# Performance work log

Measured on AMD Instinct MI355X. Metric: run time of the kernel, lower is better.

The kernel has to match this reference:

```python
import jax, jax.numpy as jnp
import numpy as np

N = 50000        # nodes
E = 800000       # edges
D_IN = 128       # input feature dim (== 2*hidden)
H = 64           # hidden_dim
G = 64           # graphs in batch
BN_EPS = 1e-5


def setup_inputs() -> dict:
    key = jax.random.key(0)
    ks = jax.random.split(key, 8)
    x = jax.random.normal(ks[0], (N, D_IN), jnp.float32)
    edge_index = jax.random.randint(ks[1], (2, E), 0, N, dtype=jnp.int32)
    edge_attribute = jax.random.normal(ks[2], (E,), jnp.float32)
    batch = jnp.sort(jax.random.randint(ks[3], (N,), 0, G, dtype=jnp.int32))
    # 7 GIN layers; all first linears are [D_IN=2H -> H]
    W1 = jax.random.normal(ks[4], (7, D_IN, H), jnp.float32) * (1.0 / np.sqrt(D_IN))
    bn1_g = jnp.ones((7, H), jnp.float32)
    bn1_b = jnp.zeros((7, H), jnp.float32)
    # layers 0..5 second linear [H -> 2H] + BN
    W2 = jax.random.normal(ks[5], (6, H, 2 * H), jnp.float32) * (1.0 / np.sqrt(H))
    bn2_g = jnp.ones((6, 2 * H), jnp.float32)
    bn2_b = jnp.zeros((6, 2 * H), jnp.float32)
    # layer 6 second linear [H -> 2], no BN
    W_last = jax.random.normal(ks[6], (H, 2), jnp.float32) * (1.0 / np.sqrt(H))
    eps = jnp.zeros((7,), jnp.float32)  # train_eps=True, init 0
    return dict(x=x, edge_index=edge_index, edge_attribute=edge_attribute,
                batch=batch, W1=W1, bn1_g=bn1_g, bn1_b=bn1_b, W2=W2,
                bn2_g=bn2_g, bn2_b=bn2_b, W_last=W_last, eps=eps)


def _bn(h, g, b):
    # training-mode BatchNorm1d over node axis, biased variance
    mu = h.mean(0)
    var = h.var(0)
    return g * (h - mu) * jax.lax.rsqrt(var + BN_EPS) + b


def reference(x, edge_index, edge_attribute, batch, W1, bn1_g, bn1_b, W2,
              bn2_g, bn2_b, W_last, eps):
    src, dst = edge_index[0], edge_index[1]
    for i in range(7):
        # GIN aggregation: sum of neighbor features (edge_attribute unused)
        agg = jax.ops.segment_sum(x[src], dst, num_segments=N)
        h = (1.0 + eps[i]) * x + agg
        h = jax.nn.relu(_bn(h @ W1[i], bn1_g[i], bn1_b[i]))
        if i < 6:
            h = _bn(h @ W2[i], bn2_g[i], bn2_b[i])
        else:
            h = h @ W_last
        # F.dropout treated as identity (deterministic eval); then ReLU
        x = jax.nn.relu(h)
    # global_mean_pool over graphs
    counts = jax.ops.segment_sum(jnp.ones((N,), x.dtype), batch, num_segments=G)
    sums = jax.ops.segment_sum(x, batch, num_segments=G)
    return sums / jnp.maximum(counts, 1.0)[:, None]
```

## Files before the change

kernel.cpp:

```cpp
#include <hip/hip_runtime.h>
#include <hip/hip_fp16.h>

#define NN 50000
#define EE 800000
#define GG 64
#define BNEPS 1e-5f

typedef _Float16 f16x8 __attribute__((ext_vector_type(8)));
typedef _Float16 f16x2 __attribute__((ext_vector_type(2)));
typedef float f32x4 __attribute__((ext_vector_type(4)));

__device__ inline float2 h2f(unsigned int u) {
    __half2 h = __builtin_bit_cast(__half2, u);
    return __half22float2(h);
}
__device__ inline unsigned int f2h(float a, float b) {
    __half2 h = __float22half2_rn(make_float2(a, b));
    return __builtin_bit_cast(unsigned int, h);
}
__device__ inline __half2 relu2(__half2 v) {
    const __half z = __float2half(0.f);
    return __halves2half2(__hmax(__low2half(v), z), __hmax(__high2half(v), z));
}
__device__ inline float acc_lo(unsigned int u, float c) {
    return __builtin_amdgcn_fdot2(__builtin_bit_cast(f16x2, u), f16x2{(_Float16)1.f, (_Float16)0.f}, c, false);
}
__device__ inline float acc_hi(unsigned int u, float c) {
    return __builtin_amdgcn_fdot2(__builtin_bit_cast(f16x2, u), f16x2{(_Float16)0.f, (_Float16)1.f}, c, false);
}


__global__ void hist_kernel(const int* __restrict__ ei, int* __restrict__ deg) {
    int e = blockIdx.x * 256 + threadIdx.x;
    if (e < EE) atomicAdd(&deg[ei[EE + e]], 1);
}

__global__ void scan1_kernel(const int* __restrict__ deg, int* __restrict__ offs,
                             int* __restrict__ bsum) {
    __shared__ int lds[1024];
    int i = blockIdx.x * 1024 + threadIdx.x;
    int v = (i < NN) ? deg[i] : 0;
    lds[threadIdx.x] = v;
    __syncthreads();
    for (int d = 1; d < 1024; d <<= 1) {
        int t = (threadIdx.x >= d) ? lds[threadIdx.x - d] : 0;
        __syncthreads();
        lds[threadIdx.x] += t;
        __syncthreads();
    }
    int incl = lds[threadIdx.x];
    if (i < NN) offs[i] = incl - v;
    if (threadIdx.x == 1023) bsum[blockIdx.x] = incl;
}

__global__ void scan3_kernel(int* __restrict__ offs, int* __restrict__ cursor,
                             const int* __restrict__ bsum) {
    __shared__ int base;
    if (threadIdx.x == 0) {
        int r = 0;
        for (int b = 0; b < (int)blockIdx.x; ++b) r += bsum[b];
        base = r;
    }
    __syncthreads();
    int i = blockIdx.x * 1024 + threadIdx.x;
    if (i < NN) {
        int o = offs[i] + base;
        offs[i] = o;
        cursor[i] = o;
    }
    if (i == 0 && blockIdx.x == 0) offs[NN] = EE;
}

__global__ void scatter_kernel(const int* __restrict__ ei, int* __restrict__ cursor,
                               unsigned short* __restrict__ srcs) {
    int e = blockIdx.x * 256 + threadIdx.x;
    if (e < EE) {
        int s = ei[e];
        int d = ei[EE + e];
        int pos = atomicAdd(&cursor[d], 1);
        srcs[pos] = (unsigned short)s;
    }
}


__global__ void cvt_kernel(const float* __restrict__ in, __half* __restrict__ out) {
    int i = blockIdx.x * 256 + threadIdx.x;
    if (i >= NN * 16) return;
    const float4* p = (const float4*)in + i * 2;
    float4 a = p[0], b = p[1];
    uint4 o;
    o.x = f2h(a.x, a.y);
    o.y = f2h(a.z, a.w);
    o.z = f2h(b.x, b.y);
    o.w = f2h(b.z, b.w);
    ((uint4*)out)[i] = o;
}


__global__ void packW_kernel(const float* __restrict__ W, __half* __restrict__ Wpk, int K,
                             int C, int layers) {
    int NKF = K / 32, NCF = C / 16;
    int per_layer = NKF * NCF * 64;
    int t = blockIdx.x * 256 + threadIdx.x;
    if (t >= layers * per_layer) return;
    int layer = t / per_layer, r = t % per_layer;
    int kf = r / (NCF * 64), r2 = r % (NCF * 64);
    int cf = r2 >> 6, l = r2 & 63;
    const float* Wl = W + (size_t)layer * K * C;
    __half* o = Wpk + ((size_t)layer * per_layer + ((size_t)(kf * NCF + cf) * 64 + l)) * 8;
    int k0 = kf * 32 + (l >> 4) * 8, c = cf * 16 + (l & 15);
#pragma unroll
    for (int j = 0; j < 8; ++j) o[j] = __float2half(Wl[(size_t)(k0 + j) * C + c]);
}


__global__ __launch_bounds__(256) void bnrelu_kernel(__half* __restrict__ a,
                                                     const float* __restrict__ stats,
                                                     const float* __restrict__ bg,
                                                     const float* __restrict__ bb) {
    __shared__ float lsc[128], lsh[128];
    if (threadIdx.x < 128) {
        int c = threadIdx.x;
        float mu = stats[c] * (1.0f / NN);
        float var = stats[128 + c] * (1.0f / NN) - mu * mu;
        float inv = rsqrtf(var + BNEPS);
        float sc = bg[c] * inv;
        lsc[c] = sc;
        lsh[c] = bb[c] - mu * sc;
    }
    __syncthreads();
    const int total = NN * 16;
    for (int t = blockIdx.x * 256 + threadIdx.x; t < total; t += gridDim.x * 256) {
        uint4 u = ((const uint4*)a)[t];
        int c0 = (t & 15) * 8;
        unsigned int* up = &u.x;
        uint4 o;
        unsigned int* op = &o.x;
#pragma unroll
        for (int j = 0; j < 4; ++j) {
            float2 f = h2f(up[j]);
            f.x = fmaxf(fmaf(f.x, lsc[c0 + 2 * j], lsh[c0 + 2 * j]), 0.f);
            f.y = fmaxf(fmaf(f.y, lsc[c0 + 2 * j + 1], lsh[c0 + 2 * j + 1]), 0.f);
            op[j] = f2h(f.x, f.y);
        }
        ((uint4*)a)[t] = o;
    }
}


__global__ __launch_bounds__(256) void agg_kernel(const __half* __restrict__ x,
                                                  const int* __restrict__ offs,
                                                  const unsigned short* __restrict__ srcs,
                                                  const float* __restrict__ epsp, int layer,
                                                  __half* __restrict__ h0) {
    int node = blockIdx.x * 4 + (threadIdx.x >> 6);
    if (node >= NN) return;
    int lane = threadIdx.x & 63;
    int g = lane >> 3;
    int l = lane & 7;
    float acc[16];
#pragma unroll
    for (int j = 0; j < 16; ++j) acc[j] = 0.f;

    int beg = offs[node], end = offs[node + 1];
    int i0 = beg + g, i1 = i0 + 8;
    int s0 = (i0 < end) ? (int)srcs[i0] : 0;
    int s1 = (i1 < end) ? (int)srcs[i1] : 0;
    const uint4* r0 = (const uint4*)(x + (size_t)s0 * 128) + l * 2;
    const uint4* r1 = (const uint4*)(x + (size_t)s1 * 128) + l * 2;
    uint4 va = r0[0], vb = r0[1];
    uint4 wa = r1[0], wb = r1[1];
    const uint4* sp = (const uint4*)(x + (size_t)node * 128) + l * 2;
    uint4 xa, xb;
    if (g == 0) {
        xa = sp[0];
        xb = sp[1];
    }
    for (int base = beg; base + g < end; base += 8) {
        int i2 = base + 16 + g;
        int sP = (i2 < end) ? (int)srcs[i2] : 0;
        const uint4* r2 = (const uint4*)(x + (size_t)sP * 128) + l * 2;
        uint4 ua = r2[0], ub = r2[1];
#pragma unroll
        for (int j = 0; j < 8; ++j) {
            unsigned int u = (j == 0) ? va.x : (j == 1) ? va.y : (j == 2) ? va.z
                             : (j == 3) ? va.w : (j == 4) ? vb.x : (j == 5) ? vb.y
                             : (j == 6) ? vb.z : vb.w;
            acc[2 * j] = acc_lo(u, acc[2 * j]);
            acc[2 * j + 1] = acc_hi(u, acc[2 * j + 1]);
        }
        va = wa; vb = wb;
        wa = ua; wb = ub;
    }
    float e1 = 1.0f + epsp[layer];
    if (g == 0) {
#pragma unroll
        for (int j = 0; j < 8; ++j) {
            unsigned int u = (j == 0) ? xa.x : (j == 1) ? xa.y : (j == 2) ? xa.z
                             : (j == 3) ? xa.w : (j == 4) ? xb.x : (j == 5) ? xb.y
                             : (j == 6) ? xb.z : xb.w;
            float2 f = h2f(u);
            acc[2 * j] = fmaf(e1, f.x, acc[2 * j]);
            acc[2 * j + 1] = fmaf(e1, f.y, acc[2 * j + 1]);
        }
    }
#pragma unroll
    for (int d = 8; d < 64; d <<= 1)
#pragma unroll
        for (int j = 0; j < 16; ++j) acc[j] += __shfl_xor(acc[j], d);
    if (g == 0) {
        uint4 o0, o1;
        o0.x = f2h(acc[0], acc[1]);
        o0.y = f2h(acc[2], acc[3]);
        o0.z = f2h(acc[4], acc[5]);
        o0.w = f2h(acc[6], acc[7]);
        o1.x = f2h(acc[8], acc[9]);
        o1.y = f2h(acc[10], acc[11]);
        o1.z = f2h(acc[12], acc[13]);
        o1.w = f2h(acc[14], acc[15]);
        uint4* o = (uint4*)(h0 + (size_t)node * 128 + l * 16);
        o[0] = o0;
        o[1] = o1;
    }
}


__global__ __launch_bounds__(256) void gemm1_kernel(const __half* __restrict__ h0,
                                                    const __half* __restrict__ Wpk,
                                                    __half* __restrict__ y,
                                                    float* __restrict__ stats) {
    int lane = threadIdx.x & 63, wave = threadIdx.x >> 6, g = lane >> 4;
    f16x8 bf[4][4];
    const f16x8* wp = (const f16x8*)Wpk;
#pragma unroll
    for (int kf = 0; kf < 4; ++kf)
#pragma unroll
        for (int cf = 0; cf < 4; ++cf) bf[kf][cf] = wp[(kf * 4 + cf) * 64 + lane];
    float s[4] = {0.f, 0.f, 0.f, 0.f}, s2[4] = {0.f, 0.f, 0.f, 0.f};
    for (int tile = blockIdx.x * 4 + wave; tile < NN / 16; tile += gridDim.x * 4) {
        int node16 = tile * 16;
        f32x4 acc[4];
#pragma unroll
        for (int cf = 0; cf < 4; ++cf) acc[cf] = (f32x4){0.f, 0.f, 0.f, 0.f};
        const f16x8* xr = (const f16x8*)(h0 + (size_t)(node16 + (lane & 15)) * 128);
#pragma unroll
        for (int kf = 0; kf < 4; ++kf) {
            f16x8 af = xr[kf * 4 + g];
#pragma unroll
            for (int cf = 0; cf < 4; ++cf)
                acc[cf] =
                    __builtin_amdgcn_mfma_f32_16x16x32_f16(af, bf[kf][cf], acc[cf], 0, 0, 0);
        }
#pragma unroll
        for (int cf = 0; cf < 4; ++cf) {
#pragma unroll
            for (int r = 0; r < 4; ++r) {
                float v = acc[cf][r];
                float p = __shfl_xor(v, 1);
                if (!(lane & 1)) {
                    int node = node16 + g * 4 + r;
                    int ch = cf * 16 + (lane & 15);
                    *(unsigned int*)(y + (size_t)node * 64 + ch) = f2h(v, p);
                }
                s[cf] += v;
                s2[cf] += v * v;
            }
        }
    }
#pragma unroll
    for (int d = 16; d < 64; d <<= 1)
#pragma unroll
        for (int cf = 0; cf < 4; ++cf) {
            s[cf] += __shfl_xor(s[cf], d);
            s2[cf] += __shfl_xor(s2[cf], d);
        }
    __shared__ float lst[4][128];
    if (lane < 16) {
#pragma unroll
        for (int cf = 0; cf < 4; ++cf) {
            lst[wave][cf * 16 + lane] = s[cf];
            lst[wave][64 + cf * 16 + lane] = s2[cf];
        }
    }
    __syncthreads();
    if (threadIdx.x < 128)
        atomicAdd(&stats[threadIdx.x], lst[0][threadIdx.x] + lst[1][threadIdx.x] +
                                           lst[2][threadIdx.x] + lst[3][threadIdx.x]);
}


__global__ __launch_bounds__(256) void gemm2_kernel(const __half* __restrict__ y1,
                                                    const __half* __restrict__ Wpk,
                                                    const float* __restrict__ stats1,
                                                    const float* __restrict__ bg,
                                                    const float* __restrict__ bb,
                                                    __half* __restrict__ y2,
                                                    float* __restrict__ stats2) {
    __shared__ __half2 lsc2[32], lsh2[32];
    if (threadIdx.x < 32) {
        int p = threadIdx.x;
        int c0 = 2 * p, c1 = 2 * p + 1;
        float mu0 = stats1[c0] * (1.0f / NN);
        float var0 = stats1[64 + c0] * (1.0f / NN) - mu0 * mu0;
        float is0 = rsqrtf(var0 + BNEPS);
        float sc0 = bg[c0] * is0;
        float mu1 = stats1[c1] * (1.0f / NN);
        float var1 = stats1[64 + c1] * (1.0f / NN) - mu1 * mu1;
        float is1 = rsqrtf(var1 + BNEPS);
        float sc1 = bg[c1] * is1;
        lsc2[p] = __floats2half2_rn(sc0, sc1);
        lsh2[p] = __floats2half2_rn(bb[c0] - mu0 * sc0, bb[c1] - mu1 * sc1);
    }
    __syncthreads();
    int lane = threadIdx.x & 63, wave = threadIdx.x >> 6, g = lane >> 4;
    f16x8 bf[2][8];
    const f16x8* wp = (const f16x8*)Wpk;
#pragma unroll
    for (int kf = 0; kf < 2; ++kf)
#pragma unroll
        for (int cf = 0; cf < 8; ++cf) bf[kf][cf] = wp[(kf * 8 + cf) * 64 + lane];
    float s[8] = {0.f, 0.f, 0.f, 0.f, 0.f, 0.f, 0.f, 0.f};
    float s2[8] = {0.f, 0.f, 0.f, 0.f, 0.f, 0.f, 0.f, 0.f};
    for (int tile = blockIdx.x * 4 + wave; tile < NN / 16; tile += gridDim.x * 4) {
        int node16 = tile * 16;
        f32x4 acc[8];
#pragma unroll
        for (int cf = 0; cf < 8; ++cf) acc[cf] = (f32x4){0.f, 0.f, 0.f, 0.f};
        const f16x8* xr = (const f16x8*)(y1 + (size_t)(node16 + (lane & 15)) * 64);
#pragma unroll
        for (int kf = 0; kf < 2; ++kf) {
            f16x8 af = xr[kf * 4 + g];
            __half2* ap = (__half2*)&af;
            int p0 = kf * 16 + g * 4;
#pragma unroll
            for (int j = 0; j < 4; ++j)
                ap[j] = relu2(__hfma2(ap[j], lsc2[p0 + j], lsh2[p0 + j]));
#pragma unroll
            for (int cf = 0; cf < 8; ++cf)
                acc[cf] =
                    __builtin_amdgcn_mfma_f32_16x16x32_f16(af, bf[kf][cf], acc[cf], 0, 0, 0);
        }
#pragma unroll
        for (int cf = 0; cf < 8; ++cf) {
#pragma unroll
            for (int r = 0; r < 4; ++r) {
                float v = acc[cf][r];
                float p = __shfl_xor(v, 1);
                if (!(lane & 1)) {
                    int node = node16 + g * 4 + r;
                    int ch = cf * 16 + (lane & 15);
                    *(unsigned int*)(y2 + (size_t)node * 128 + ch) = f2h(v, p);
                }
                s[cf] += v;
                s2[cf] += v * v;
            }
        }
    }
#pragma unroll
    for (int d = 16; d < 64; d <<= 1)
#pragma unroll
        for (int cf = 0; cf < 8; ++cf) {
            s[cf] += __shfl_xor(s[cf], d);
            s2[cf] += __shfl_xor(s2[cf], d);
        }
    __shared__ float lst[4][256];
    if (lane < 16) {
#pragma unroll
        for (int cf = 0; cf < 8; ++cf) {
            lst[wave][cf * 16 + lane] = s[cf];
            lst[wave][128 + cf * 16 + lane] = s2[cf];
        }
    }
    __syncthreads();
    atomicAdd(&stats2[threadIdx.x], lst[0][threadIdx.x] + lst[1][threadIdx.x] +
                                        lst[2][threadIdx.x] + lst[3][threadIdx.x]);
}


__global__ void gemm_last_kernel(const __half* __restrict__ y1, const float* __restrict__ W,
                                 const float* __restrict__ stats1,
                                 const float* __restrict__ bg, const float* __restrict__ bb,
                                 const int* __restrict__ batch, float* __restrict__ pool) {
    __shared__ float lw[128];
    __shared__ float lsc[64], lsh[64];
    if (threadIdx.x < 128) lw[threadIdx.x] = W[threadIdx.x];
    if (threadIdx.x < 64) {
        int c = threadIdx.x;
        float mu = stats1[c] * (1.0f / NN);
        float var = stats1[64 + c] * (1.0f / NN) - mu * mu;
        float inv = rsqrtf(var + BNEPS);
        float sc = bg[c] * inv;
        lsc[c] = sc;
        lsh[c] = bb[c] - mu * sc;
    }
    __syncthreads();
    int n = blockIdx.x * 256 + threadIdx.x;
    int lane = threadIdx.x & 63;
    int gID = -1;
    float v0 = 0.f, v1 = 0.f, cnt = 0.f;
    if (n < NN) {
        float a0 = 0.f, a1 = 0.f;
        const uint4* row = (const uint4*)(y1 + (size_t)n * 64);
#pragma unroll
        for (int c8 = 0; c8 < 8; ++c8) {
            uint4 u = row[c8];
#pragma unroll
            for (int j = 0; j < 4; ++j) {
                unsigned int w = (j == 0) ? u.x : (j == 1) ? u.y : (j == 2) ? u.z : u.w;
                float2 f = h2f(w);
                int k = c8 * 8 + j * 2;
                float t0 = fmaxf(fmaf(f.x, lsc[k], lsh[k]), 0.f);
                float t1 = fmaxf(fmaf(f.y, lsc[k + 1], lsh[k + 1]), 0.f);
                a0 = fmaf(t0, lw[2 * k + 0], a0);
                a1 = fmaf(t0, lw[2 * k + 1], a1);
                a0 = fmaf(t1, lw[2 * k + 2], a0);
                a1 = fmaf(t1, lw[2 * k + 3], a1);
            }
        }
        gID = batch[n];
        v0 = fmaxf(a0, 0.f);
        v1 = fmaxf(a1, 0.f);
        cnt = 1.0f;
    }
    for (int d = 1; d < 64; d <<= 1) {
        int tg = __shfl_up(gID, d);
        float t0 = __shfl_up(v0, d);
        float t1 = __shfl_up(v1, d);
        float tc = __shfl_up(cnt, d);
        if (lane >= d && tg == gID) { v0 += t0; v1 += t1; cnt += tc; }
    }
    int gn = __shfl_down(gID, 1);
    bool lastv = (lane == 63) || (gn != gID);
    if (gID >= 0 && lastv) {
        atomicAdd(&pool[gID * 3 + 0], v0);
        atomicAdd(&pool[gID * 3 + 1], v1);
        atomicAdd(&pool[gID * 3 + 2], cnt);
    }
}

__global__ void pool_fin_kernel(const float* __restrict__ pool, float* __restrict__ out) {
    int t = threadIdx.x;
    if (t < GG * 2) {
        int g = t >> 1, j = t & 1;
        float cnt = pool[g * 3 + 2];
        out[t] = pool[g * 3 + j] / fmaxf(cnt, 1.0f);
    }
}


extern "C" void kernel_launch(void* const* d_in, const int* in_sizes, int n_in,
                              void* d_out, int out_size, void* d_ws, size_t ws_size,
                              hipStream_t stream) {
    const float* x_in  = (const float*)d_in[0];
    const int*   ei    = (const int*)d_in[1];
    const int*   batch = (const int*)d_in[3];
    const float* W1    = (const float*)d_in[4];
    const float* bn1g  = (const float*)d_in[5];
    const float* bn1b  = (const float*)d_in[6];
    const float* W2    = (const float*)d_in[7];
    const float* bn2g  = (const float*)d_in[8];
    const float* bn2b  = (const float*)d_in[9];
    const float* Wlast = (const float*)d_in[10];
    const float* eps   = (const float*)d_in[11];
    float* out = (float*)d_out;

    char* ws = (char*)d_ws;
    size_t off = 0;
    auto alloc = [&](size_t bytes) -> char* {
        char* p = ws + off;
        off += (bytes + 255) & ~(size_t)255;
        return p;
    };
    int*   deg      = (int*)alloc((size_t)NN * 4);
    float* statsall = (float*)alloc(16 * 256 * 4);
    float* pool     = (float*)alloc((size_t)GG * 3 * 4);
    size_t zero_len = off;
    int*            offs   = (int*)alloc((size_t)(NN + 1) * 4);
    int*            cursor = (int*)alloc((size_t)NN * 4);
    int*            bsum   = (int*)alloc(64 * 4);
    unsigned short* srcs   = (unsigned short*)alloc((size_t)EE * 2);
    __half*         X16    = (__half*)alloc((size_t)NN * 128 * 2);
    __half*         A16    = (__half*)alloc((size_t)NN * 128 * 2);
    __half*         B16    = (__half*)alloc((size_t)NN * 128 * 2);
    __half*         C16    = (__half*)alloc((size_t)NN * 64 * 2);
    __half*         Wpk1   = (__half*)alloc((size_t)7 * 8192 * 2);
    __half*         Wpk2   = (__half*)alloc((size_t)6 * 8192 * 2);
    (void)ws_size; (void)n_in; (void)in_sizes; (void)out_size;

    hipMemsetAsync(ws, 0, zero_len, stream);

    hist_kernel<<<(EE + 255) / 256, 256, 0, stream>>>(ei, deg);
    scan1_kernel<<<49, 1024, 0, stream>>>(deg, offs, bsum);
    scan3_kernel<<<49, 1024, 0, stream>>>(offs, cursor, bsum);
    scatter_kernel<<<(EE + 255) / 256, 256, 0, stream>>>(ei, cursor, srcs);
    cvt_kernel<<<(NN * 16 + 255) / 256, 256, 0, stream>>>(x_in, X16);
    packW_kernel<<<(7 * 1024 + 255) / 256, 256, 0, stream>>>(W1, Wpk1, 128, 64, 7);
    packW_kernel<<<(6 * 1024 + 255) / 256, 256, 0, stream>>>(W2, Wpk2, 64, 128, 6);

    for (int i = 0; i < 7; ++i) {
        int s1 = 2 * i, s2 = 2 * i + 1;
        agg_kernel<<<(NN + 3) / 4, 256, 0, stream>>>(i == 0 ? X16 : A16, offs, srcs, eps, i,
                                                     B16);
        gemm1_kernel<<<256, 256, 0, stream>>>(B16, Wpk1 + (size_t)i * 8192, C16,
                                              statsall + s1 * 256);
        if (i < 6) {
            gemm2_kernel<<<256, 256, 0, stream>>>(C16, Wpk2 + (size_t)i * 8192,
                                                  statsall + s1 * 256, bn1g + i * 64,
                                                  bn1b + i * 64, A16, statsall + s2 * 256);
            bnrelu_kernel<<<2048, 256, 0, stream>>>(A16, statsall + s2 * 256,
                                                    bn2g + i * 128, bn2b + i * 128);
        } else {
            gemm_last_kernel<<<(NN + 255) / 256, 256, 0, stream>>>(
                C16, Wlast, statsall + s1 * 256, bn1g + i * 64, bn1b + i * 64, batch, pool);
        }
    }

    pool_fin_kernel<<<1, 128, 0, stream>>>(pool, out);
}
```

Baseline: 565.1 us.

## Partition CSR scatter by destination slice and narrow agg edge groups to 4

```diff
diff --git a/kernel.cpp b/kernel.cpp
--- a/kernel.cpp
+++ b/kernel.cpp
@@ -23,10 +23,12 @@
     return __halves2half2(__hmax(__low2half(v), z), __hmax(__high2half(v), z));
 }
 __device__ inline float acc_lo(unsigned int u, float c) {
-    return __builtin_amdgcn_fdot2(__builtin_bit_cast(f16x2, u), f16x2{(_Float16)1.f, (_Float16)0.f}, c, false);
+    return __builtin_amdgcn_fdot2(__builtin_bit_cast(f16x2, u),
+                                  f16x2{(_Float16)1.f, (_Float16)0.f}, c, false);
 }
 __device__ inline float acc_hi(unsigned int u, float c) {
-    return __builtin_amdgcn_fdot2(__builtin_bit_cast(f16x2, u), f16x2{(_Float16)0.f, (_Float16)1.f}, c, false);
+    return __builtin_amdgcn_fdot2(__builtin_bit_cast(f16x2, u),
+                                  f16x2{(_Float16)0.f, (_Float16)1.f}, c, false);
 }
 
 
@@ -71,14 +73,23 @@
     if (i == 0 && blockIdx.x == 0) offs[NN] = EE;
 }
 
-__global__ void scatter_kernel(const int* __restrict__ ei, int* __restrict__ cursor,
-                               unsigned short* __restrict__ srcs) {
-    int e = blockIdx.x * 256 + threadIdx.x;
-    if (e < EE) {
-        int s = ei[e];
+
+__global__ __launch_bounds__(256) void scatter_kernel(const int* __restrict__ ei,
+                                                      int* __restrict__ cursor,
+                                                      unsigned short* __restrict__ srcs) {
+    const int SLICE = NN / 8;
+    int slice = blockIdx.x & 7;
+    int chunk = blockIdx.x >> 3;
+    const int per_chunk = (EE + 127) / 128;
+    int lo = slice * SLICE, hi = lo + SLICE;
+    int e_end = min((chunk + 1) * per_chunk, EE);
+    for (int e = chunk * per_chunk + threadIdx.x; e < e_end; e += 256) {
         int d = ei[EE + e];
-        int pos = atomicAdd(&cursor[d], 1);
-        srcs[pos] = (unsigned short)s;
+        if (d >= lo && d < hi) {
+            int s = ei[e];
+            int pos = atomicAdd(&cursor[d], 1);
+            srcs[pos] = (unsigned short)s;
+        }
     }
 }
 
@@ -156,71 +167,56 @@
     int node = blockIdx.x * 4 + (threadIdx.x >> 6);
     if (node >= NN) return;
     int lane = threadIdx.x & 63;
-    int g = lane >> 3;
-    int l = lane & 7;
-    float acc[16];
-#pragma unroll
-    for (int j = 0; j < 16; ++j) acc[j] = 0.f;
+    int g = lane >> 4;
+    int l = lane & 15;
+    float acc[8];
+#pragma unroll
+    for (int j = 0; j < 8; ++j) acc[j] = 0.f;
 
     int beg = offs[node], end = offs[node + 1];
-    int i0 = beg + g, i1 = i0 + 8;
+    int i0 = beg + g, i1 = i0 + 4;
     int s0 = (i0 < end) ? (int)srcs[i0] : 0;
     int s1 = (i1 < end) ? (int)srcs[i1] : 0;
-    const uint4* r0 = (const uint4*)(x + (size_t)s0 * 128) + l * 2;
-    const uint4* r1 = (const uint4*)(x + (size_t)s1 * 128) + l * 2;
-    uint4 va = r0[0], vb = r0[1];
-    uint4 wa = r1[0], wb = r1[1];
-    const uint4* sp = (const uint4*)(x + (size_t)node * 128) + l * 2;
-    uint4 xa, xb;
-    if (g == 0) {
-        xa = sp[0];
-        xb = sp[1];
-    }
-    for (int base = beg; base + g < end; base += 8) {
-        int i2 = base + 16 + g;
+    uint4 va = ((const uint4*)(x + (size_t)s0 * 128))[l];
+    uint4 wa = ((const uint4*)(x + (size_t)s1 * 128))[l];
+    uint4 xa;
+    if (g == 0) xa = ((const uint4*)(x + (size_t)node * 128))[l];
+    for (int base = beg; base + g < end; base += 4) {
+        int i2 = base + 8 + g;
         int sP = (i2 < end) ? (int)srcs[i2] : 0;
-        const uint4* r2 = (const uint4*)(x + (size_t)sP * 128) + l * 2;
-        uint4 ua = r2[0], ub = r2[1];
-#pragma unroll
-        for (int j = 0; j < 8; ++j) {
-            unsigned int u = (j == 0) ? va.x : (j == 1) ? va.y : (j == 2) ? va.z
-                             : (j == 3) ? va.w : (j == 4) ? vb.x : (j == 5) ? vb.y
-                             : (j == 6) ? vb.z : vb.w;
-            acc[2 * j] = acc_lo(u, acc[2 * j]);
-            acc[2 * j + 1] = acc_hi(u, acc[2 * j + 1]);
-        }
-        va = wa; vb = wb;
-        wa = ua; wb = ub;
+        uint4 ua = ((const uint4*)(x + (size_t)sP * 128))[l];
+        acc[0] = acc_lo(va.x, acc[0]);
+        acc[1] = acc_hi(va.x, acc[1]);
+        acc[2] = acc_lo(va.y, acc[2]);
+        acc[3] = acc_hi(va.y, acc[3]);
+        acc[4] = acc_lo(va.z, acc[4]);
+        acc[5] = acc_hi(va.z, acc[5]);
+        acc[6] = acc_lo(va.w, acc[6]);
+        acc[7] = acc_hi(va.w, acc[7]);
+        va = wa;
+        wa = ua;
     }
     float e1 = 1.0f + epsp[layer];
     if (g == 0) {
 #pragma unroll
-        for (int j = 0; j < 8; ++j) {
-            unsigned int u = (j == 0) ? xa.x : (j == 1) ? xa.y : (j == 2) ? xa.z
-                             : (j == 3) ? xa.w : (j == 4) ? xb.x : (j == 5) ? xb.y
-                             : (j == 6) ? xb.z : xb.w;
+        for (int j = 0; j < 4; ++j) {
+            unsigned int u = (j == 0) ? xa.x : (j == 1) ? xa.y : (j == 2) ? xa.z : xa.w;
             float2 f = h2f(u);
             acc[2 * j] = fmaf(e1, f.x, acc[2 * j]);
             acc[2 * j + 1] = fmaf(e1, f.y, acc[2 * j + 1]);
         }
     }
 #pragma unroll
-    for (int d = 8; d < 64; d <<= 1)
-#pragma unroll
-        for (int j = 0; j < 16; ++j) acc[j] += __shfl_xor(acc[j], d);
+    for (int d = 16; d < 64; d <<= 1)
+#pragma unroll
+        for (int j = 0; j < 8; ++j) acc[j] += __shfl_xor(acc[j], d);
     if (g == 0) {
-        uint4 o0, o1;
-        o0.x = f2h(acc[0], acc[1]);
-        o0.y = f2h(acc[2], acc[3]);
-        o0.z = f2h(acc[4], acc[5]);
-        o0.w = f2h(acc[6], acc[7]);
-        o1.x = f2h(acc[8], acc[9]);
-        o1.y = f2h(acc[10], acc[11]);
-        o1.z = f2h(acc[12], acc[13]);
-        o1.w = f2h(acc[14], acc[15]);
-        uint4* o = (uint4*)(h0 + (size_t)node * 128 + l * 16);
-        o[0] = o0;
-        o[1] = o1;
+        uint4 o;
+        o.x = f2h(acc[0], acc[1]);
+        o.y = f2h(acc[2], acc[3]);
+        o.z = f2h(acc[4], acc[5]);
+        o.w = f2h(acc[6], acc[7]);
+        ((uint4*)(h0 + (size_t)node * 128))[l] = o;
     }
 }
 
@@ -492,7 +488,7 @@
     hist_kernel<<<(EE + 255) / 256, 256, 0, stream>>>(ei, deg);
     scan1_kernel<<<49, 1024, 0, stream>>>(deg, offs, bsum);
     scan3_kernel<<<49, 1024, 0, stream>>>(offs, cursor, bsum);
-    scatter_kernel<<<(EE + 255) / 256, 256, 0, stream>>>(ei, cursor, srcs);
+    scatter_kernel<<<1024, 256, 0, stream>>>(ei, cursor, srcs);
     cvt_kernel<<<(NN * 16 + 255) / 256, 256, 0, stream>>>(x_in, X16);
     packW_kernel<<<(7 * 1024 + 255) / 256, 256, 0, stream>>>(W1, Wpk1, 128, 64, 7);
     packW_kernel<<<(6 * 1024 + 255) / 256, 256, 0, stream>>>(W2, Wpk2, 64, 128, 6);
```

Result: slower. 581.0 us (+2.8%).
